# Kernel optimization log

Hardware: AMD Instinct MI355X
Metric: run time of the kernel (lower is better)

Reference implementation:

```python
import jax, jax.numpy as jnp
import numpy as np

B, C, H, W = 4, 32, 64, 64
K = 3
HEADS = 8
SF = 4
D = C * K * K          # 288, unfold token dim
E = D // 2             # 144, reduced dim
DH = E // HEADS        # 18, head dim
SCALE = DH ** -0.5
N = H * W              # 4096 tokens


def unfold(x):
    # x: (B,C,H,W) -> (B, C*K*K, H*W), torch.nn.Unfold ordering (c, kh, kw)
    xp = jnp.pad(x, ((0, 0), (0, 0), (1, 1), (1, 1)))
    patches = jnp.stack([xp[:, :, i:i + H, j:j + W] for i in range(K) for j in range(K)], axis=2)
    return patches.reshape(x.shape[0], C * K * K, H * W)


def fold(cols):
    # inverse of unfold: scatter-add overlapping patches back, crop padding
    b = cols.shape[0]
    y = cols.reshape(b, C, K, K, H, W)
    out = jnp.zeros((b, C, H + 2, W + 2), cols.dtype)
    for i in range(K):
        for j in range(K):
            out = out.at[:, :, i:i + H, j:j + W].add(y[:, :, i, j])
    return out[:, :, 1:-1, 1:-1]


def layernorm_cols(cols, g, b):
    # LayerNorm over D applied on (B,N,D) view, returned as (B,D,N)
    xt = cols.transpose(0, 2, 1)
    mu = xt.mean(-1, keepdims=True)
    var = xt.var(-1, keepdims=True)
    y = (xt - mu) / jnp.sqrt(var + 1e-5) * g + b
    return y.transpose(0, 2, 1)


def emha(x, wr, br, wqkv, we, be):
    # x: (B, D, N)
    b, _, n_tok = x.shape
    xr = jnp.einsum('bdn,ed->ben', x, wr) + br[None, :, None]   # Conv1d k=1 reduction
    t = xr.transpose(0, 2, 1)                                   # (B,N,E)
    qkv = t @ wqkv.T                                            # Linear, no bias
    q, k, v = jnp.split(qkv, 3, axis=-1)
    n = n_tok // SF

    def rs(a):
        return a.reshape(b, n_tok, HEADS, DH).transpose(0, 2, 1, 3).reshape(b, HEADS, SF, n, DH)

    q, k, v = rs(q), rs(k), rs(v)
    attn = jax.nn.softmax(jnp.einsum('bhsnd,bhsmd->bhsnm', q, k) * SCALE, axis=-1)
    o = jnp.einsum('bhsnm,bhsmd->bhsnd', attn, v)
    o = o.reshape(b, HEADS, n_tok, DH).transpose(0, 2, 1, 3).reshape(b, n_tok, E).transpose(0, 2, 1)
    return jnp.einsum('ben,fe->bfn', o, we) + be[None, :, None]  # Conv1d k=1 expansion


def conv3x3(x, w, b):
    y = jax.lax.conv_general_dilated(x, w, (1, 1), ((1, 1), (1, 1)),
                                     dimension_numbers=('NCHW', 'OIHW', 'NCHW'))
    return y + b[None, :, None, None]


def setup_inputs() -> dict:
    key = jax.random.key(0)
    ks = jax.random.split(key, 20)
    s = 0.02
    inp = {
        'x': jax.random.normal(ks[0], (B, C, H, W), jnp.float32),
        'ln_g': jnp.ones((D,), jnp.float32),
        'ln_b': jnp.zeros((D,), jnp.float32),
        'conv_w': jax.random.normal(ks[1], (C, C, 3, 3), jnp.float32) * s,
        'conv_b': jnp.zeros((C,), jnp.float32),
    }
    for i in range(3):
        k0, k1, k2 = jax.random.split(ks[2 + i], 3)
        inp[f'wr{i+1}'] = jax.random.normal(k0, (E, D), jnp.float32) * s
        inp[f'br{i+1}'] = jnp.zeros((E,), jnp.float32)
        inp[f'wqkv{i+1}'] = jax.random.normal(k1, (3 * E, E), jnp.float32) * s
        inp[f'we{i+1}'] = jax.random.normal(k2, (D, E), jnp.float32) * s
        inp[f'be{i+1}'] = jnp.zeros((D,), jnp.float32)
    return inp


def reference(x, ln_g, ln_b, conv_w, conv_b,
              wr1, br1, wqkv1, we1, be1,
              wr2, br2, wqkv2, we2, be2,
              wr3, br3, wqkv3, we3, be3):
    t = x
    for (wr, br, wqkv, we, be) in ((wr1, br1, wqkv1, we1, be1),
                                   (wr2, br2, wqkv2, we2, be2),
                                   (wr3, br3, wqkv3, we3, be3)):
        cols = unfold(t)
        cols_n = layernorm_cols(cols, ln_g, ln_b)
        cols = emha(cols_n, wr, br, wqkv, we, be) + cols
        t = fold(cols)
    return x + jax.nn.elu(conv3x3(t, conv_w, conv_b))
```

## Files before the change

kernel.cpp:

```cpp
#include <hip/hip_runtime.h>
#include <math.h>

#define BN 4
#define CC 32
#define HH 64
#define WW 64
#define DD 288
#define EE 144
#define NTOK 4096
#define SCALE_F 0.2357022603955158f
#define QSCALE  0.3401074286f
#define QKST 384
#define MQKV 528

typedef __bf16 bf16x8 __attribute__((ext_vector_type(8)));
typedef float floatx4 __attribute__((ext_vector_type(4)));
typedef unsigned short u16x8 __attribute__((ext_vector_type(8)));

__device__ __forceinline__ unsigned short f2bf(float x) {
    unsigned int u = __float_as_uint(x);
    u += 0x7fffu + ((u >> 16) & 1u);
    return (unsigned short)(u >> 16);
}
__device__ __forceinline__ float bf2f(unsigned short s) {
    return __uint_as_float(((unsigned int)s) << 16);
}
__device__ __forceinline__ unsigned int pack_bf_trunc(float a, float b) {
    return __builtin_amdgcn_perm(__float_as_uint(b), __float_as_uint(a), 0x07060302u);
}

__global__ __launch_bounds__(256) void setup_k(
    const float* __restrict__ wr0, const float* __restrict__ br0,
    const float* __restrict__ wr1, const float* __restrict__ br1,
    const float* __restrict__ wr2, const float* __restrict__ br2,
    const float* __restrict__ g,  const float* __restrict__ lb,
    const float* __restrict__ wqkv0, const float* __restrict__ wqkv1, const float* __restrict__ wqkv2,
    const float* __restrict__ we0,   const float* __restrict__ we1,   const float* __restrict__ we2,
    unsigned short* __restrict__ wg_bf, float* __restrict__ wgsum, float* __restrict__ wbeta,
    unsigned short* __restrict__ wqkv_bf, unsigned short* __restrict__ we_bf)
{
    int blk = blockIdx.x;
    int tid = threadIdx.x;
    if (blk < 3) {
        if (tid < 144) {
            int l = blk, e = tid;
            const float* wr = (l == 0) ? wr0 : ((l == 1) ? wr1 : wr2);
            const float* br = (l == 0) ? br0 : ((l == 1) ? br1 : br2);
            float sg = 0.f, sb = 0.f;
            for (int d = 0; d < DD; ++d) {
                float w = wr[e * DD + d];
                float wgv = w * g[d];
                wg_bf[((size_t)l * EE + e) * DD + d] = f2bf(wgv);
                sg += wgv;
                sb += w * lb[d];
            }
            wgsum[l * EE + e] = sg;
            wbeta[l * EE + e] = sb + br[e];
        }
        return;
    }
    int idx = (blk - 3) * 256 + tid;
    const int T1 = 3 * MQKV * 160;
    const int T2 = 3 * 288 * 160;
    if (idx < T1) {
        int l = idx / (MQKV * 160), r = idx % (MQKV * 160);
        int m = r / 160, k = r % 160;
        const float* w = (l == 0) ? wqkv0 : ((l == 1) ? wqkv1 : wqkv2);
        float v = 0.f;
        if (k < 144) {
            if (m < 192) {
                int h = m / 24, j = m % 24;
                if (j < 18) v = w[(h * 18 + j) * 144 + k] * QSCALE;
            } else if (m < 384) {
                int mm = m - 192, h = mm / 24, j = mm % 24;
                if (j < 18) v = w[(144 + h * 18 + j) * 144 + k];
            } else {
                v = w[(288 + (m - 384)) * 144 + k];
            }
        }
        wqkv_bf[idx] = f2bf(v);
    } else if (idx < T1 + T2) {
        int j = idx - T1;
        int l = j / (288 * 160), r = j % (288 * 160);
        int m = r / 160, k = r % 160;
        const float* w = (l == 0) ? we0 : ((l == 1) ? we1 : we2);
        we_bf[j] = (k < 144) ? f2bf(w[m * 144 + k]) : 0;
    }
}

__global__ __launch_bounds__(256) void unfold_k(const float* __restrict__ t,
    unsigned short* __restrict__ colsT,
    float* __restrict__ mu, float* __restrict__ rstd)
{
    __shared__ float red1[4][64], red2[4][64];
    int tid = threadIdx.x;
    int lane = tid & 63, cpart = tid >> 6;
    int b = blockIdx.x >> 6, nc = blockIdx.x & 63;
    int n = nc * 64 + lane;
    int h = n >> 6, w = n & 63;
    const float* tb = t + (size_t)b * CC * HH * WW;
    unsigned short loc[72];
    float s1 = 0.f, s2 = 0.f;
    #pragma unroll
    for (int c8 = 0; c8 < 8; ++c8) {
        int c = cpart * 8 + c8;
        const float* tc = tb + (size_t)c * 4096;
        #pragma unroll
        for (int i = 0; i < 3; ++i) {
            int hr = h + i - 1;
            bool rok = ((unsigned)hr < 64u);
            #pragma unroll
            for (int j = 0; j < 3; ++j) {
                int wc = w + j - 1;
                bool ok = rok && ((unsigned)wc < 64u);
                float v = ok ? tc[hr * 64 + wc] : 0.f;
                loc[c8 * 9 + i * 3 + j] = f2bf(v);
                s1 += v;
                s2 = fmaf(v, v, s2);
            }
        }
    }
    unsigned short* ct = colsT + ((size_t)b * NTOK + n) * 288 + cpart * 72;
    #pragma unroll
    for (int u = 0; u < 9; ++u)
        *(u16x8*)&ct[u * 8] = *(const u16x8*)&loc[u * 8];
    red1[cpart][lane] = s1;
    red2[cpart][lane] = s2;
    __syncthreads();
    if (tid < 64) {
        float a = red1[0][tid] + red1[1][tid] + red1[2][tid] + red1[3][tid];
        float q = red2[0][tid] + red2[1][tid] + red2[2][tid] + red2[3][tid];
        float m = a * (1.f / 288.f);
        float var = q * (1.f / 288.f) - m * m;
        int nn = nc * 64 + tid;
        mu[b * NTOK + nn] = m;
        rstd[b * NTOK + nn] = rsqrtf(var + 1e-5f);
    }
}

template<int K, int MODE, int NYB>
__global__ __launch_bounds__(256) void mgemm_k(
    const unsigned short* __restrict__ A, const unsigned short* __restrict__ Bt, int BST,
    unsigned short* __restrict__ Ct, unsigned short* __restrict__ Cv,
    const float* __restrict__ mu, const float* __restrict__ rstd,
    const float* __restrict__ wgsum, const float* __restrict__ wbeta,
    const float* __restrict__ bias)
{
    constexpr int NT = 64;
    __shared__ unsigned short Ts[64 * 56];
    int flat = blockIdx.x;
    int g  = (flat / (8 * NYB)) * 8 + (flat & 7);
    int jm = (flat % (8 * NYB)) >> 3;
    int n0 = (g & 63) * NT;
    int bI = g >> 6;
    int m0 = jm * 48;
    int tid = threadIdx.x;
    int wv = tid >> 6, lane = tid & 63;
    int l15 = lane & 15, l4 = lane >> 4;

    const unsigned short* Arow = A + (size_t)(m0 + l15) * K + l4 * 8;
    const unsigned short* Brow = Bt + ((size_t)bI * NTOK + n0 + wv * 16 + l15) * BST + l4 * 8;

    floatx4 acc[3];
    acc[0] = acc[1] = acc[2] = (floatx4){0.f, 0.f, 0.f, 0.f};

    #pragma unroll
    for (int ks = 0; ks < K / 32; ++ks) {
        bf16x8 bfr = *(const bf16x8*)(Brow + ks * 32);
        #pragma unroll
        for (int mi = 0; mi < 3; ++mi) {
            bf16x8 af = *(const bf16x8*)(Arow + (size_t)mi * 16 * K + ks * 32);
            acc[mi] = __builtin_amdgcn_mfma_f32_16x16x32_bf16(af, bfr, acc[mi], 0, 0, 0);
        }
    }

    int n_l = wv * 16 + l15;

    if (MODE == 2) {
        #pragma unroll
        for (int mi = 0; mi < 3; ++mi)
            #pragma unroll
            for (int r = 0; r < 4; ++r) {
                int m_l = mi * 16 + l4 * 4 + r;
                Ts[m_l * 72 + n_l] = f2bf(acc[mi][r] + bias[m0 + m_l]);
            }
        __syncthreads();
        for (int u = tid; u < 48 * 8; u += 256) {
            int row = u >> 3, seg = u & 7;
            unsigned short* dst = Ct + ((size_t)bI * DD + m0 + row) * NTOK + n0 + seg * 8;
            *(u16x8*)dst = *(const u16x8*)&Ts[row * 72 + seg * 8];
        }
    } else {
        bool vpath = (MODE == 0) && (m0 >= 384);
        float muv = 0.f, rsv = 0.f;
        if (MODE == 1) {
            int n_g = n0 + n_l;
            muv = mu[bI * NTOK + n_g];
            rsv = rstd[bI * NTOK + n_g];
        }
        #pragma unroll
        for (int mi = 0; mi < 3; ++mi)
            #pragma unroll
            for (int r = 0; r < 4; ++r) {
                int m_l = mi * 16 + l4 * 4 + r;
                float v = acc[mi][r];
                if (MODE == 1) v = rsv * (v - muv * wgsum[m0 + m_l]) + wbeta[m0 + m_l];
                if (!vpath) Ts[n_l * 56 + m_l] = f2bf(v);
                else        Ts[m_l * 72 + n_l] = f2bf(v);
            }
        __syncthreads();
        if (!vpath) {
            const int CTS = (MODE == 1) ? 160 : QKST;
            if (tid < 128) {
                int row = tid >> 1, half = tid & 1;
                unsigned short* dst = Ct + ((size_t)bI * NTOK + n0 + row) * CTS + m0 + half * 24;
                const unsigned short* src = &Ts[row * 56 + half * 24];
                #pragma unroll
                for (int u = 0; u < 3; ++u)
                    *(u16x8*)&dst[u * 8] = *(const u16x8*)&src[u * 8];
                if (MODE == 1 && m0 == 96) {
                    u16x8 z = (u16x8)0;
                    *(u16x8*)(Ct + ((size_t)bI * NTOK + n0 + row) * 160 + 144 + half * 8) = z;
                }
            }
        } else {
            for (int u = tid; u < 48 * 8; u += 256) {
                int row = u >> 3, seg = u & 7;
                unsigned short* dst = Cv + ((size_t)bI * EE + (m0 - 384) + row) * NTOK + n0 + seg * 8;
                *(u16x8*)dst = *(const u16x8*)&Ts[row * 72 + seg * 8];
            }
        }
    }
}

__global__ __launch_bounds__(256) void attn_k2(const unsigned short* __restrict__ qkT,
                                               const unsigned short* __restrict__ vF,
                                               unsigned short* __restrict__ oT)
{
    __shared__ unsigned short Ks[128 * 40];
    __shared__ unsigned short Vs[32 * 136];
    __shared__ unsigned short Ps[4 * 32 * 72];

    int blk = blockIdx.x;
    int bhs = blk & 127;
    int qc  = blk >> 7;
    int b = bhs >> 5, h = (bhs >> 2) & 7, s = bhs & 3;
    int tid  = threadIdx.x;
    int wv   = tid >> 6;
    int lane = tid & 63;
    int l15 = lane & 15, l4 = lane >> 4;
    int q0 = qc * 128;
    int tokbase = s * 1024;

    const unsigned short* qkb = qkT + (size_t)b * NTOK * QKST;

    if (tid < 128) {
        u16x8 z = (u16x8)0;
        *(u16x8*)&Ks[tid * 40 + 24] = z;
    } else {
        for (int v = tid - 128; v < 14 * 16; v += 128) {
            int d = 18 + (v >> 4), seg = v & 15;
            unsigned short val = (d == 31) ? (unsigned short)0x3F80 : (unsigned short)0;
            u16x8 vv = (u16x8)val;
            *(u16x8*)&Vs[d * 136 + seg * 8] = vv;
        }
    }

    bf16x8 qf[2];
    #pragma unroll
    for (int ni = 0; ni < 2; ++ni) {
        u16x8 raw = *(const u16x8*)(qkb + (size_t)(tokbase + q0 + wv * 32 + ni * 16 + l15) * QKST
                                    + 24 * h + l4 * 8);
        if (l4 == 3) raw = (u16x8)0;
        qf[ni] = *(bf16x8*)&raw;
    }

    floatx4 oacc[2][2];
    #pragma unroll
    for (int i = 0; i < 2; ++i)
        #pragma unroll
        for (int j = 0; j < 2; ++j)
            oacc[i][j] = (floatx4){0.f, 0.f, 0.f, 0.f};

    unsigned short* Pw = &Ps[wv * 32 * 72];

    u16x8 preg[3];
    int vb = tid - 128;
    bool v3 = (vb < 32);
    if (tid < 128) {
        const unsigned short* src = qkb + (size_t)(tokbase + tid) * QKST + 192 + 24 * h;
        preg[0] = *(const u16x8*)&src[0];
        preg[1] = *(const u16x8*)&src[8];
        preg[2] = *(const u16x8*)&src[16];
    } else {
        const unsigned short* vbb = vF + (size_t)b * EE * NTOK + tokbase;
        #pragma unroll
        for (int u = 0; u < 3; ++u) {
            int idx = vb + u * 128;
            if (u < 2 || v3) {
                int d = idx >> 4, seg = idx & 15;
                preg[u] = *(const u16x8*)(vbb + (size_t)(h * 18 + d) * NTOK + seg * 8);
            }
        }
    }

    for (int c0 = 0; c0 < 1024; c0 += 128) {
        __syncthreads();
        if (tid < 128) {
            unsigned short* dk = &Ks[tid * 40];
            *(u16x8*)&dk[0]  = preg[0];
            *(u16x8*)&dk[8]  = preg[1];
            *(u16x8*)&dk[16] = preg[2];
        } else {
            #pragma unroll
            for (int u = 0; u < 3; ++u) {
                int idx = vb + u * 128;
                if (u < 2 || v3) {
                    int d = idx >> 4, seg = idx & 15;
                    *(u16x8*)&Vs[d * 136 + seg * 8] = preg[u];
                }
            }
        }
        int cn = c0 + 128;
        if (cn < 1024) {
            if (tid < 128) {
                const unsigned short* src = qkb + (size_t)(tokbase + cn + tid) * QKST + 192 + 24 * h;
                preg[0] = *(const u16x8*)&src[0];
                preg[1] = *(const u16x8*)&src[8];
                preg[2] = *(const u16x8*)&src[16];
            } else {
                const unsigned short* vbb = vF + (size_t)b * EE * NTOK + tokbase + cn;
                #pragma unroll
                for (int u = 0; u < 3; ++u) {
                    int idx = vb + u * 128;
                    if (u < 2 || v3) {
                        int d = idx >> 4, seg = idx & 15;
                        preg[u] = *(const u16x8*)(vbb + (size_t)(h * 18 + d) * NTOK + seg * 8);
                    }
                }
            }
        }
        __syncthreads();

        #pragma unroll
        for (int sub = 0; sub < 2; ++sub) {
            bf16x8 kf[4];
            #pragma unroll
            for (int mi = 0; mi < 4; ++mi)
                kf[mi] = *(const bf16x8*)&Ks[(sub * 64 + mi * 16 + l15) * 40 + l4 * 8];

            floatx4 sacc[4][2];
            #pragma unroll
            for (int mi = 0; mi < 4; ++mi)
                #pragma unroll
                for (int ni = 0; ni < 2; ++ni) {
                    floatx4 z = (floatx4){0.f, 0.f, 0.f, 0.f};
                    sacc[mi][ni] = __builtin_amdgcn_mfma_f32_16x16x32_bf16(kf[mi], qf[ni], z, 0, 0, 0);
                }

            #pragma unroll
            for (int mi = 0; mi < 4; ++mi)
                #pragma unroll
                for (int ni = 0; ni < 2; ++ni) {
                    int ql   = ni * 16 + l15;
                    int tokb = mi * 16 + l4 * 4;
                    unsigned int lo = pack_bf_trunc(exp2f(sacc[mi][ni][0]), exp2f(sacc[mi][ni][1]));
                    unsigned int hi = pack_bf_trunc(exp2f(sacc[mi][ni][2]), exp2f(sacc[mi][ni][3]));
                    uint2 pk = make_uint2(lo, hi);
                    *(uint2*)&Pw[ql * 72 + tokb] = pk;
                }

            #pragma unroll
            for (int ks = 0; ks < 2; ++ks) {
                bf16x8 pf[2], vf[2];
                pf[0] = *(const bf16x8*)&Pw[(     l15) * 72 + ks * 32 + l4 * 8];
                pf[1] = *(const bf16x8*)&Pw[(16 + l15) * 72 + ks * 32 + l4 * 8];
                vf[0] = *(const bf16x8*)&Vs[(     l15) * 136 + sub * 64 + ks * 32 + l4 * 8];
                vf[1] = *(const bf16x8*)&Vs[(16 + l15) * 136 + sub * 64 + ks * 32 + l4 * 8];
                #pragma unroll
                for (int mi = 0; mi < 2; ++mi)
                    #pragma unroll
                    for (int nd = 0; nd < 2; ++nd)
                        oacc[mi][nd] = __builtin_amdgcn_mfma_f32_16x16x32_bf16(pf[mi], vf[nd], oacc[mi][nd], 0, 0, 0);
            }
        }
    }

    float* fO = (float*)Pw;
    #pragma unroll
    for (int mi = 0; mi < 2; ++mi)
        #pragma unroll
        for (int r = 0; r < 4; ++r) {
            float lsum = __shfl(oacc[mi][1][r], (lane & 48) | 15, 64);
            float inv  = 1.f / lsum;
            int ql = mi * 16 + l4 * 4 + r;
            fO[ql * 33 + l15] = oacc[mi][0][r] * inv;
            if (l15 < 2) fO[ql * 33 + 16 + l15] = oacc[mi][1][r] * inv;
        }

    {
        int q = lane & 31, dh = lane >> 5;
        size_t rowi = (size_t)b * NTOK + tokbase + q0 + wv * 32 + q;
        unsigned short* orow = oT + rowi * 160 + h * 18;
        for (int i = dh; i < 9; i += 2) {
            float a  = fO[q * 33 + 2 * i];
            float bb = fO[q * 33 + 2 * i + 1];
            *(unsigned int*)&orow[2 * i] = (unsigned)f2bf(a) | ((unsigned)f2bf(bb) << 16);
        }
        if (h == 7) {
            u16x8 z = (u16x8)0;
            *(u16x8*)(oT + rowi * 160 + 144 + dh * 8) = z;
        }
    }
}

__global__ __launch_bounds__(256) void fold_k(const unsigned short* __restrict__ cols,
                                              const float* __restrict__ tprev,
                                              float* __restrict__ t)
{
    int idx = blockIdx.x * 256 + threadIdx.x;
    int w = idx & 63;
    int h = (idx >> 6) & 63;
    int c = (idx >> 12) & 31;
    int b = idx >> 17;
    const unsigned short* cb = cols + (size_t)b * DD * NTOK + (size_t)c * 9 * NTOK;
    float sum = 0.f;
    #pragma unroll
    for (int i = 0; i < 3; ++i) {
        int hs = h + 1 - i;
        if ((unsigned)hs < 64u) {
            #pragma unroll
            for (int j = 0; j < 3; ++j) {
                int ws_ = w + 1 - j;
                if ((unsigned)ws_ < 64u)
                    sum += bf2f(cb[(size_t)(i * 3 + j) * NTOK + hs * 64 + ws_]);
            }
        }
    }
    int ch = (h == 0 || h == 63) ? 2 : 3;
    int cw_ = (w == 0 || w == 63) ? 2 : 3;
    t[idx] = sum + (float)(ch * cw_) * tprev[idx];
}

__global__ __launch_bounds__(256) void conv_k(const float* __restrict__ t,
    const float* __restrict__ cw, const float* __restrict__ cbias,
    const float* __restrict__ x, float* __restrict__ out)
{
    __shared__ float wsh[CC * 9];
    int blk = blockIdx.x;
    int band = blk & 3, co = (blk >> 2) & 31, b = blk >> 7;
    int tid = threadIdx.x;
    for (int u = tid; u < CC * 9; u += 256) wsh[u] = cw[co * CC * 9 + u];
    __syncthreads();
    int h = band * 16 + (tid >> 4);
    int w0 = (tid & 15) << 2;
    const float* tb = t + (size_t)b * CC * 4096;
    float bias = cbias[co];
    float a0 = bias, a1 = bias, a2 = bias, a3 = bias;
    for (int ci = 0; ci < CC; ++ci) {
        const float* tc = tb + (size_t)ci * 4096;
        const float* wr = &wsh[ci * 9];
        #pragma unroll
        for (int i = 0; i < 3; ++i) {
            int hr = h + i - 1;
            if ((unsigned)hr < 64u) {
                const float* row = tc + hr * 64;
                float vl = (w0 > 0)  ? row[w0 - 1] : 0.f;
                float4 c4 = *(const float4*)&row[w0];
                float vr = (w0 < 60) ? row[w0 + 4] : 0.f;
                float wj0 = wr[i * 3], wj1 = wr[i * 3 + 1], wj2 = wr[i * 3 + 2];
                a0 = fmaf(wj0, vl,   a0); a0 = fmaf(wj1, c4.x, a0); a0 = fmaf(wj2, c4.y, a0);
                a1 = fmaf(wj0, c4.x, a1); a1 = fmaf(wj1, c4.y, a1); a1 = fmaf(wj2, c4.z, a1);
                a2 = fmaf(wj0, c4.y, a2); a2 = fmaf(wj1, c4.z, a2); a2 = fmaf(wj2, c4.w, a2);
                a3 = fmaf(wj0, c4.z, a3); a3 = fmaf(wj1, c4.w, a3); a3 = fmaf(wj2, vr,   a3);
            }
        }
    }
    size_t oidx = ((size_t)(b * CC + co) * 4096) + h * 64 + w0;
    float4 xin = *(const float4*)&x[oidx];
    float4 o;
    o.x = xin.x + ((a0 > 0.f) ? a0 : (__expf(a0) - 1.f));
    o.y = xin.y + ((a1 > 0.f) ? a1 : (__expf(a1) - 1.f));
    o.z = xin.z + ((a2 > 0.f) ? a2 : (__expf(a2) - 1.f));
    o.w = xin.w + ((a3 > 0.f) ? a3 : (__expf(a3) - 1.f));
    *(float4*)&out[oidx] = o;
}

extern "C" void kernel_launch(void* const* d_in, const int* in_sizes, int n_in,
                              void* d_out, int out_size, void* d_ws, size_t ws_size,
                              hipStream_t stream)
{
    const float* x    = (const float*)d_in[0];
    const float* ln_g = (const float*)d_in[1];
    const float* ln_b = (const float*)d_in[2];
    const float* cw   = (const float*)d_in[3];
    const float* cb   = (const float*)d_in[4];
    const float* wr[3]   = {(const float*)d_in[5],  (const float*)d_in[10], (const float*)d_in[15]};
    const float* br[3]   = {(const float*)d_in[6],  (const float*)d_in[11], (const float*)d_in[16]};
    const float* wqkv[3] = {(const float*)d_in[7],  (const float*)d_in[12], (const float*)d_in[17]};
    const float* we[3]   = {(const float*)d_in[8],  (const float*)d_in[13], (const float*)d_in[18]};
    const float* be[3]   = {(const float*)d_in[9],  (const float*)d_in[14], (const float*)d_in[19]};
    float* out = (float*)d_out;

    char* p = (char*)d_ws;
    unsigned short* cols_bf = (unsigned short*)p; p += (size_t)BN * DD * NTOK * 2;
    unsigned short* colsT = (unsigned short*)p; p += (size_t)BN * NTOK * 288 * 2;
    unsigned short* oT = colsT;
    unsigned short* xrT   = (unsigned short*)p; p += (size_t)BN * NTOK * 160 * 2;
    unsigned short* qkT   = (unsigned short*)p; p += (size_t)BN * NTOK * QKST * 2;
    unsigned short* vF    = (unsigned short*)p; p += (size_t)BN * EE * NTOK * 2;
    float* mu   = (float*)p;              p += (size_t)BN * NTOK * 4;
    float* rstd = (float*)p;              p += (size_t)BN * NTOK * 4;
    float* tA   = (float*)p;              p += (size_t)BN * CC * HH * WW * 4;
    float* tB   = (float*)p;              p += (size_t)BN * CC * HH * WW * 4;
    unsigned short* wg_bf   = (unsigned short*)p; p += (size_t)3 * EE * DD * 2;
    unsigned short* wqkv_bf = (unsigned short*)p; p += (size_t)3 * MQKV * 160 * 2;
    unsigned short* we_bf   = (unsigned short*)p; p += (size_t)3 * DD * 160 * 2;
    float* wgsum = (float*)p;             p += 3 * EE * 4;
    float* wbeta = (float*)p;             p += 3 * EE * 4;
    (void)in_sizes; (void)n_in; (void)out_size; (void)ws_size;

    setup_k<<<1533, 256, 0, stream>>>(wr[0], br[0], wr[1], br[1], wr[2], br[2], ln_g, ln_b,
                                      wqkv[0], wqkv[1], wqkv[2], we[0], we[1], we[2],
                                      wg_bf, wgsum, wbeta, wqkv_bf, we_bf);

    const float* tin = x;
    float* touts[3] = {tA, tB, tA};
    for (int l = 0; l < 3; ++l) {
        unfold_k<<<256, 256, 0, stream>>>(tin, colsT, mu, rstd);
        mgemm_k<288, 1, 3><<<768, 256, 0, stream>>>(
            wg_bf + (size_t)l * EE * DD, colsT, 288, xrT, nullptr,
            mu, rstd, wgsum + l * EE, wbeta + l * EE, nullptr);
        mgemm_k<160, 0, 11><<<2816, 256, 0, stream>>>(
            wqkv_bf + (size_t)l * MQKV * 160, xrT, 160, qkT, vF,
            nullptr, nullptr, nullptr, nullptr, nullptr);
        attn_k2<<<1024, 256, 0, stream>>>(qkT, vF, oT);
        mgemm_k<160, 2, 6><<<1536, 256, 0, stream>>>(
            we_bf + (size_t)l * DD * 160, oT, 160, cols_bf, nullptr,
            nullptr, nullptr, nullptr, nullptr, be[l]);
        fold_k<<<2048, 256, 0, stream>>>(cols_bf, tin, touts[l]);
        tin = touts[l];
    }
    conv_k<<<512, 256, 0, stream>>>(tA, cw, cb, x, out);
}
```

Measured before the change: 444.1 us.

## Keep attention probabilities in registers via permlane swaps, halve query tile

The attention kernel no longer stages exp'd scores through shared memory. It rearranges the S accumulator fragments into the PV MFMA operand layout with v_permlane32/16_swap and writes the output directly from registers. Each block now handles 64 queries (16 per wave) with twice as many blocks, and launch bounds request 6 waves per SIMD for occupancy. This removes the LDS round trip for P and the fO staging, but K/V loads are now amortized over fewer queries per block.

```diff
diff --git a/kernel.cpp b/kernel.cpp
--- a/kernel.cpp
+++ b/kernel.cpp
@@ -27,6 +27,12 @@
 }
 __device__ __forceinline__ unsigned int pack_bf_trunc(float a, float b) {
     return __builtin_amdgcn_perm(__float_as_uint(b), __float_as_uint(a), 0x07060302u);
+}
+__device__ __forceinline__ void plswap32(unsigned int& a, unsigned int& b) {
+    asm("v_permlane32_swap_b32 %0, %1" : "+v"(a), "+v"(b));
+}
+__device__ __forceinline__ void plswap16(unsigned int& a, unsigned int& b) {
+    asm("v_permlane16_swap_b32 %0, %1" : "+v"(a), "+v"(b));
 }
 
 __global__ __launch_bounds__(256) void setup_k(
@@ -233,13 +239,12 @@
     }
 }
 
-__global__ __launch_bounds__(256) void attn_k2(const unsigned short* __restrict__ qkT,
-                                               const unsigned short* __restrict__ vF,
-                                               unsigned short* __restrict__ oT)
+__global__ __launch_bounds__(256, 6) void attn_k2(const unsigned short* __restrict__ qkT,
+                                                  const unsigned short* __restrict__ vF,
+                                                  unsigned short* __restrict__ oT)
 {
     __shared__ unsigned short Ks[128 * 40];
     __shared__ unsigned short Vs[32 * 136];
-    __shared__ unsigned short Ps[4 * 32 * 72];
 
     int blk = blockIdx.x;
     int bhs = blk & 127;
@@ -249,7 +254,7 @@
     int wv   = tid >> 6;
     int lane = tid & 63;
     int l15 = lane & 15, l4 = lane >> 4;
-    int q0 = qc * 128;
+    int q0 = qc * 64;
     int tokbase = s * 1024;
 
     const unsigned short* qkb = qkT + (size_t)b * NTOK * QKST;
@@ -266,23 +271,17 @@
         }
     }
 
-    bf16x8 qf[2];
-    #pragma unroll
-    for (int ni = 0; ni < 2; ++ni) {
-        u16x8 raw = *(const u16x8*)(qkb + (size_t)(tokbase + q0 + wv * 32 + ni * 16 + l15) * QKST
+    bf16x8 qf;
+    {
+        u16x8 raw = *(const u16x8*)(qkb + (size_t)(tokbase + q0 + wv * 16 + l15) * QKST
                                     + 24 * h + l4 * 8);
         if (l4 == 3) raw = (u16x8)0;
-        qf[ni] = *(bf16x8*)&raw;
-    }
-
-    floatx4 oacc[2][2];
-    #pragma unroll
-    for (int i = 0; i < 2; ++i)
-        #pragma unroll
-        for (int j = 0; j < 2; ++j)
-            oacc[i][j] = (floatx4){0.f, 0.f, 0.f, 0.f};
-
-    unsigned short* Pw = &Ps[wv * 32 * 72];
+        qf = *(bf16x8*)&raw;
+    }
+
+    floatx4 oacc[2];
+    oacc[0] = (floatx4){0.f, 0.f, 0.f, 0.f};
+    oacc[1] = (floatx4){0.f, 0.f, 0.f, 0.f};
 
     u16x8 preg[3];
     int vb = tid - 128;
@@ -349,68 +348,52 @@
             for (int mi = 0; mi < 4; ++mi)
                 kf[mi] = *(const bf16x8*)&Ks[(sub * 64 + mi * 16 + l15) * 40 + l4 * 8];
 
-            floatx4 sacc[4][2];
-            #pragma unroll
-            for (int mi = 0; mi < 4; ++mi)
+            floatx4 sacc[4];
+            #pragma unroll
+            for (int mi = 0; mi < 4; ++mi) {
+                floatx4 z = (floatx4){0.f, 0.f, 0.f, 0.f};
+                sacc[mi] = __builtin_amdgcn_mfma_f32_16x16x32_bf16(kf[mi], qf, z, 0, 0, 0);
+            }
+
+            unsigned int pk0[4], pk1[4];
+            #pragma unroll
+            for (int mi = 0; mi < 4; ++mi) {
+                pk0[mi] = pack_bf_trunc(exp2f(sacc[mi][0]), exp2f(sacc[mi][1]));
+                pk1[mi] = pack_bf_trunc(exp2f(sacc[mi][2]), exp2f(sacc[mi][3]));
+            }
+
+            #pragma unroll
+            for (int c = 0; c < 2; ++c) {
+                unsigned int B0 = pk0[2 * c], B2 = pk0[2 * c + 1];
+                unsigned int B1 = pk1[2 * c], B3 = pk1[2 * c + 1];
+                plswap32(B0, B2); plswap16(B0, B2);
+                plswap32(B1, B3); plswap16(B1, B3);
+                union { unsigned int u[4]; bf16x8 v; } bfr;
+                bfr.u[0] = B0; bfr.u[1] = B1; bfr.u[2] = B2; bfr.u[3] = B3;
                 #pragma unroll
-                for (int ni = 0; ni < 2; ++ni) {
-                    floatx4 z = (floatx4){0.f, 0.f, 0.f, 0.f};
-                    sacc[mi][ni] = __builtin_amdgcn_mfma_f32_16x16x32_bf16(kf[mi], qf[ni], z, 0, 0, 0);
+                for (int nd = 0; nd < 2; ++nd) {
+                    bf16x8 af = *(const bf16x8*)&Vs[(nd * 16 + l15) * 136 + sub * 64 + c * 32 + l4 * 8];
+                    oacc[nd] = __builtin_amdgcn_mfma_f32_16x16x32_bf16(af, bfr.v, oacc[nd], 0, 0, 0);
                 }
-
-            #pragma unroll
-            for (int mi = 0; mi < 4; ++mi)
-                #pragma unroll
-                for (int ni = 0; ni < 2; ++ni) {
-                    int ql   = ni * 16 + l15;
-                    int tokb = mi * 16 + l4 * 4;
-                    unsigned int lo = pack_bf_trunc(exp2f(sacc[mi][ni][0]), exp2f(sacc[mi][ni][1]));
-                    unsigned int hi = pack_bf_trunc(exp2f(sacc[mi][ni][2]), exp2f(sacc[mi][ni][3]));
-                    uint2 pk = make_uint2(lo, hi);
-                    *(uint2*)&Pw[ql * 72 + tokb] = pk;
-                }
-
-            #pragma unroll
-            for (int ks = 0; ks < 2; ++ks) {
-                bf16x8 pf[2], vf[2];
-                pf[0] = *(const bf16x8*)&Pw[(     l15) * 72 + ks * 32 + l4 * 8];
-                pf[1] = *(const bf16x8*)&Pw[(16 + l15) * 72 + ks * 32 + l4 * 8];
-                vf[0] = *(const bf16x8*)&Vs[(     l15) * 136 + sub * 64 + ks * 32 + l4 * 8];
-                vf[1] = *(const bf16x8*)&Vs[(16 + l15) * 136 + sub * 64 + ks * 32 + l4 * 8];
-                #pragma unroll
-                for (int mi = 0; mi < 2; ++mi)
-                    #pragma unroll
-                    for (int nd = 0; nd < 2; ++nd)
-                        oacc[mi][nd] = __builtin_amdgcn_mfma_f32_16x16x32_bf16(pf[mi], vf[nd], oacc[mi][nd], 0, 0, 0);
-            }
-        }
-    }
-
-    float* fO = (float*)Pw;
-    #pragma unroll
-    for (int mi = 0; mi < 2; ++mi)
-        #pragma unroll
-        for (int r = 0; r < 4; ++r) {
-            float lsum = __shfl(oacc[mi][1][r], (lane & 48) | 15, 64);
-            float inv  = 1.f / lsum;
-            int ql = mi * 16 + l4 * 4 + r;
-            fO[ql * 33 + l15] = oacc[mi][0][r] * inv;
-            if (l15 < 2) fO[ql * 33 + 16 + l15] = oacc[mi][1][r] * inv;
-        }
-
-    {
-        int q = lane & 31, dh = lane >> 5;
-        size_t rowi = (size_t)b * NTOK + tokbase + q0 + wv * 32 + q;
-        unsigned short* orow = oT + rowi * 160 + h * 18;
-        for (int i = dh; i < 9; i += 2) {
-            float a  = fO[q * 33 + 2 * i];
-            float bb = fO[q * 33 + 2 * i + 1];
-            *(unsigned int*)&orow[2 * i] = (unsigned)f2bf(a) | ((unsigned)f2bf(bb) << 16);
-        }
-        if (h == 7) {
-            u16x8 z = (u16x8)0;
-            *(u16x8*)(oT + rowi * 160 + 144 + dh * 8) = z;
-        }
+            }
+        }
+    }
+
+    float lsum = __shfl(oacc[1][3], 48 + l15, 64);
+    float inv  = 1.f / lsum;
+    size_t rowi = (size_t)b * NTOK + tokbase + q0 + wv * 16 + l15;
+    unsigned short* orow = oT + rowi * 160 + h * 18;
+    unsigned int w0 = (unsigned)f2bf(oacc[0][0] * inv) | ((unsigned)f2bf(oacc[0][1] * inv) << 16);
+    unsigned int w1 = (unsigned)f2bf(oacc[0][2] * inv) | ((unsigned)f2bf(oacc[0][3] * inv) << 16);
+    *(unsigned int*)&orow[l4 * 4]     = w0;
+    *(unsigned int*)&orow[l4 * 4 + 2] = w1;
+    if (l4 == 0) {
+        unsigned int w2 = (unsigned)f2bf(oacc[1][0] * inv) | ((unsigned)f2bf(oacc[1][1] * inv) << 16);
+        *(unsigned int*)&orow[16] = w2;
+    }
+    if (h == 7 && l4 < 2) {
+        u16x8 z = (u16x8)0;
+        *(u16x8*)(oT + rowi * 160 + 144 + l4 * 8) = z;
     }
 }
 
@@ -534,7 +517,7 @@
         mgemm_k<160, 0, 11><<<2816, 256, 0, stream>>>(
             wqkv_bf + (size_t)l * MQKV * 160, xrT, 160, qkT, vF,
             nullptr, nullptr, nullptr, nullptr, nullptr);
-        attn_k2<<<1024, 256, 0, stream>>>(qkT, vF, oT);
+        attn_k2<<<2048, 256, 0, stream>>>(qkT, vF, oT);
         mgemm_k<160, 2, 6><<<1536, 256, 0, stream>>>(
             we_bf + (size_t)l * DD * 160, oT, 160, cols_bf, nullptr,
             nullptr, nullptr, nullptr, nullptr, be[l]);
```

Measured after the change: 432.1 us. 2.7% less time.
